# Performance work log

Hardware: AMD Instinct MI355X
Metric: run time of the kernel (lower is better)

## Reference

```python
import jax, jax.numpy as jnp
import numpy as np

NB, NC, NT = 64, 128, 6
NEURON = (25, 50, 100)
AXIS = 4
EPS = 1e-12


def _offdiag_idx(nc):
    # static [nc, nc-1] column indices of the off-diagonal entries per row
    idx = np.tile(np.arange(nc)[None, :], (nc, 1))
    mask = ~np.eye(nc, dtype=bool)
    return idx[mask].reshape(nc, nc - 1)


def setup_inputs() -> dict:
    key = jax.random.key(0)
    ks = jax.random.split(key, 8)
    P = NT * NT
    coords = jax.random.normal(ks[0], (NB, NC, 3), dtype=jnp.float32)
    atom_types = jax.random.randint(ks[1], (NC,), 0, NT)
    dims = [1] + list(NEURON)
    inp = {"coords": coords, "atom_types": atom_types}
    for i in range(3):
        bound = 1.0 / float(np.sqrt(dims[i]))
        inp[f"W{i+1}"] = jax.random.uniform(ks[2 + 2 * i], (P, dims[i + 1], dims[i]), jnp.float32, -bound, bound)
        inp[f"b{i+1}"] = jax.random.uniform(ks[3 + 2 * i], (P, dims[i + 1]), jnp.float32, -bound, bound)
    return inp


def _channel_dense(x, W, b, channels, res_mode):
    # x: [nb, Ppairs, in]; W[channels]: [Ppairs, out, in] (redundant per-pair gather, as in torch)
    y = jnp.einsum('bpi,poi->bpo', x, W[channels]) + b[channels]
    y = jnp.tanh(y)
    if res_mode == 1:
        y = y + x
    elif res_mode == 2:
        y = y + jnp.concatenate([x, x], axis=-1)
    return y


def _forward(coords, atom_types, W1, b1, W2, b2, W3, b3):
    nb, nc, _ = coords.shape
    idx = jnp.asarray(_offdiag_idx(nc))  # [nc, nc-1], static
    row = jnp.arange(nc)[:, None]

    rij = coords[:, :, None, :] - coords[:, None, :, :]          # [nb,nc,nc,3]
    rij = rij[:, row, idx]                                       # [nb,nc,nc-1,3] off-diagonal
    dij = jnp.linalg.norm(rij, axis=-1)                          # [nb,nc,nc-1]
    dinv = 1.0 / jnp.maximum(dij, EPS)
    loc_env_r = dinv
    loc_env_a = rij * (dinv * dinv)[..., None]                   # [nb,nc,nc-1,3]

    neighbor_types = atom_types[idx]                             # [nc,nc-1]
    channels = (atom_types[:, None] * NT + neighbor_types).reshape(-1)  # [nc*(nc-1)]

    x = loc_env_r.reshape(nb, -1, 1)                             # [nb,P,1]
    y = _channel_dense(x, W1, b1, channels, res_mode=0)          # 1 -> 25
    y = _channel_dense(y, W2, b2, channels, res_mode=2)          # 25 -> 50 (+concat res)
    y = _channel_dense(y, W3, b3, channels, res_mode=2)          # 50 -> 100 (+concat res)

    out = y.reshape(nb, nc, nc - 1, NEURON[-1])                  # [nb,nc,k,100]
    t1 = jnp.einsum('bnka,bnkf->bnaf', loc_env_a, out[..., :AXIS])   # [nb,nc,3,4]
    t2 = jnp.einsum('bnka,bnaf->bnkf', loc_env_a, t1)                # [nb,nc,k,4]
    res = jnp.einsum('bnkg,bnkf->bngf', out, t2)                     # [nb,nc,100,4]
    return res.reshape(nb, nc, -1)


def reference(coords, atom_types, W1, b1, W2, b2, W3, b3):
    return _forward(coords, atom_types, W1, b1, W2, b2, W3, b3)
```

## Files before the change

kernel.cpp:

```cpp
#include <hip/hip_runtime.h>

#define NBATCH 64
#define NCH    128
#define NTYPE  6
#define NK     127
#define N1     25
#define N2     50
#define N3     100
#define NAXIS  4
#define OUTPER 400
#define W2P    28
#define MAXKP  152
#define MAXC4  38

#define R5(M)  M(0) M(1) M(2) M(3) M(4)
#define R7(M)  M(0) M(1) M(2) M(3) M(4) M(5) M(6)
#define R12(M) M(0) M(1) M(2) M(3) M(4) M(5) M(6) M(7) M(8) M(9) M(10) M(11)
#define R25(M) M(0) M(1) M(2) M(3) M(4) M(5) M(6) M(7) M(8) M(9) M(10) M(11) M(12) \
               M(13) M(14) M(15) M(16) M(17) M(18) M(19) M(20) M(21) M(22) M(23) M(24)
#define R25A(M,a) M(a,0) M(a,1) M(a,2) M(a,3) M(a,4) M(a,5) M(a,6) M(a,7) M(a,8) M(a,9) \
               M(a,10) M(a,11) M(a,12) M(a,13) M(a,14) M(a,15) M(a,16) M(a,17) M(a,18) \
               M(a,19) M(a,20) M(a,21) M(a,22) M(a,23) M(a,24)
#define R50(M) R25(M) M(25) M(26) M(27) M(28) M(29) M(30) M(31) M(32) M(33) M(34) \
               M(35) M(36) M(37) M(38) M(39) M(40) M(41) M(42) M(43) M(44) M(45) \
               M(46) M(47) M(48) M(49)

__device__ __forceinline__ float tanh_fast(float x) {
    float e = __expf(2.0f * x);
    return 1.0f - 2.0f * __builtin_amdgcn_rcpf(e + 1.0f);
}

__global__ void k_transpose(const float* __restrict__ coords, float* __restrict__ ct) {
    int t = blockIdx.x * blockDim.x + threadIdx.x;
    if (t >= NBATCH * NCH * 3) return;
    int b  = t & (NBATCH - 1);
    int jd = t >> 6;
    int d  = jd % 3;
    int j  = jd / 3;
    ct[t] = coords[(b * NCH + j) * 3 + d];
}

__device__ __forceinline__ void sort_k_by_type(
    const int* __restrict__ types, int n, int* tysh, int* ks, int* bins, int tid, int nthr)
{
    for (int t = tid; t < NCH; t += nthr) tysh[t] = types[t];
    __syncthreads();
    if (tid == 0) {
        for (int t = 0; t < NTYPE; ++t) bins[t] = 0;
        for (int k = 0; k < NK; ++k) { int j = (k < n) ? k : k + 1; bins[tysh[j]]++; }
        int off = 0;
        for (int t = 0; t < NTYPE; ++t) { int c = bins[t]; bins[t] = off; off += c; }
        for (int k = 0; k < NK; ++k) { int j = (k < n) ? k : k + 1; ks[bins[tysh[j]]++] = k; }
    }
    __syncthreads();
}

__device__ __forceinline__ void sort_pad(
    const int* __restrict__ types, int n, int* tysh, int* ksp, int* chs, int* aux,
    int tid, int nthr)
{
    for (int t = tid; t < NCH; t += nthr) tysh[t] = types[t];
    __syncthreads();
    if (tid == 0) {
        int cnt[NTYPE], pos[NTYPE];
        for (int t = 0; t < NTYPE; ++t) cnt[t] = 0;
        for (int k = 0; k < NK; ++k) { int j = (k < n) ? k : k + 1; cnt[tysh[j]]++; }
        int c = 0;
        for (int t = 0; t < NTYPE; ++t) {
            pos[t] = c;
            int pc = (cnt[t] + 3) & ~3;
            for (int q = c >> 2; q < (c + pc) >> 2; ++q) chs[q] = t;
            for (int p = c + cnt[t]; p < c + pc; ++p) ksp[p] = -1;
            c += pc;
        }
        aux[0] = c >> 2;
        for (int k = 0; k < NK; ++k) { int j = (k < n) ? k : k + 1; ksp[pos[tysh[j]]++] = k; }
    }
    __syncthreads();
}

__global__ __launch_bounds__(256, 4) void k_mlp(
    const float* __restrict__ ct, const int* __restrict__ types,
    const float* __restrict__ W1, const float* __restrict__ B1,
    const float* __restrict__ W2, const float* __restrict__ B2,
    const float* __restrict__ W3, const float* __restrict__ B3,
    float* __restrict__ t1buf)
{
    __shared__ int ks[NK];
    __shared__ int tysh[NCH];
    __shared__ int bins[NTYPE];

    const int n  = blockIdx.x >> 2;
    const int qc = blockIdx.x & 3;
    const int w  = threadIdx.x >> 6;
    const int b  = threadIdx.x & 63;
    const int k0 = qc * 32 + w * 8;

    sort_k_by_type(types, n, tysh, ks, bins, threadIdx.x, 256);

    const float cx = ct[(n*3+0)*NBATCH + b];
    const float cy = ct[(n*3+1)*NBATCH + b];
    const float cz = ct[(n*3+2)*NBATCH + b];
    const int tn = __builtin_amdgcn_readfirstlane(tysh[n]);

    float t1a[12];
#define TIN(i) t1a[i] = 0.0f;
    R12(TIN)
#undef TIN

    for (int kk = 0; kk < 8; ++kk) {
        const int kidx = k0 + kk;
        if (kidx >= NK) break;
        const int sk = __builtin_amdgcn_readfirstlane(ks[kidx]);
        const int j  = (sk < n) ? sk : sk + 1;
        const int ch = __builtin_amdgcn_readfirstlane(tn * NTYPE + tysh[j]);

        const float dx = cx - ct[(j*3+0)*NBATCH + b];
        const float dy = cy - ct[(j*3+1)*NBATCH + b];
        const float dz = cz - ct[(j*3+2)*NBATCH + b];
        const float d2 = dx*dx + dy*dy + dz*dz;
        const float dd = sqrtf(d2);
        const float dinv = __builtin_amdgcn_rcpf(fmaxf(dd, 1e-12f));
        const float di2 = dinv * dinv;
        const float ax = dx * di2, ay = dy * di2, az = dz * di2;

        const float* w1r = W1 + ch * N1;
        const float* b1r = B1 + ch * N1;
        float y1[N1];
#define L1S(o) y1[o] = tanh_fast(fmaf(dinv, w1r[o], b1r[o]));
        R25(L1S)
#undef L1S

        const float* w2r = W2 + ch * (N2 * N1);
        const float* b2r = B2 + ch * N2;
        const float* w3r = W3 + ch * (N3 * N2);
        float zf[4];
        zf[0] = B3[ch*N3+0]; zf[1] = B3[ch*N3+1];
        zf[2] = B3[ch*N3+2]; zf[3] = B3[ch*N3+3];
        float r[4];
#define MLP2I(o,i) z = fmaf(w2r[(o)*N1+(i)], y1[i], z);
#define MLP2(o) { float z = b2r[o]; R25A(MLP2I,o) \
        float y2o = tanh_fast(z) + y1[(o)%N1]; \
        if ((o) < 4) r[(o)&3] = y2o; \
        zf[0] = fmaf(w3r[0*N2+(o)], y2o, zf[0]); \
        zf[1] = fmaf(w3r[1*N2+(o)], y2o, zf[1]); \
        zf[2] = fmaf(w3r[2*N2+(o)], y2o, zf[2]); \
        zf[3] = fmaf(w3r[3*N2+(o)], y2o, zf[3]); }
        R50(MLP2)
#undef MLP2
#undef MLP2I

#define O4F(f) { float o4 = tanh_fast(zf[f]) + r[f]; \
        t1a[0+(f)] = fmaf(ax, o4, t1a[0+(f)]); \
        t1a[4+(f)] = fmaf(ay, o4, t1a[4+(f)]); \
        t1a[8+(f)] = fmaf(az, o4, t1a[8+(f)]); }
        O4F(0) O4F(1) O4F(2) O4F(3)
#undef O4F
    }

    float* dst = t1buf + (n * 12) * NBATCH + b;
#define TAT(i) atomicAdd(dst + (i) * NBATCH, t1a[i]);
    R12(TAT)
#undef TAT
}

__global__ __launch_bounds__(512, 3) void k_res2(
    const float* __restrict__ ct, const int* __restrict__ types,
    const float* __restrict__ W1, const float* __restrict__ B1,
    const float* __restrict__ W2, const float* __restrict__ B2,
    const float* __restrict__ W3, const float* __restrict__ B3,
    const float* __restrict__ t1buf, float* __restrict__ out)
{
    __shared__ float y2t[4 * N2 * NBATCH];
    __shared__ float t2s[4 * NBATCH * NAXIS];
    __shared__ float w2s[N2 * W2P];
    __shared__ float w1s[N1], b1s[N1], b2s[N2];
    __shared__ int   ksp[MAXKP];
    __shared__ int   chs[MAXC4];
    __shared__ int   tysh[NCH];
    __shared__ int   aux[1];

    const int n    = blockIdx.x >> 2;
    const int gh   = (blockIdx.x >> 1) & 1;
    const int kh   = blockIdx.x & 1;
    const int w    = threadIdx.x >> 6;
    const int lane = threadIdx.x & 63;
    const int kk2  = w >> 1;
    const int h    = w & 1;
    const int tid  = threadIdx.x;

    sort_pad(types, n, tysh, ksp, chs, aux, tid, 512);
    const int nch4 = __builtin_amdgcn_readfirstlane(aux[0]);
    const int c_lo = kh ? (nch4 >> 1) : 0;
    const int c_hi = kh ? nch4 : (nch4 >> 1);

    const int tn = __builtin_amdgcn_readfirstlane(tysh[n]);

    float t1r[12];
#define T1L(i) t1r[i] = t1buf[(n*12 + (i))*NBATCH + lane];
    R12(T1L)
#undef T1L

    const int g0 = __builtin_amdgcn_readfirstlane(w * 7);
    int gg[7];
#define GGI(gi) gg[gi] = ((g0 + (gi)) < N2) ? (g0 + (gi)) : (N2 - 1);
    R7(GGI)
#undef GGI

    float racc[7][4];
#define RIN(gi) racc[gi][0]=0.f; racc[gi][1]=0.f; racc[gi][2]=0.f; racc[gi][3]=0.f;
    R7(RIN)
#undef RIN

    float b3v[7];
    int prevty = -1;

    for (int kc = c_lo; kc < c_hi; ++kc) {
        const int tj = __builtin_amdgcn_readfirstlane(chs[kc]);
        const int ch = tn * NTYPE + tj;
        if (tj != prevty) {
            for (int idx = tid; idx < N2*N1; idx += 512)
                w2s[(idx / N1) * W2P + (idx % N1)] = W2[ch*(N2*N1) + idx];
            if (tid < N1) { w1s[tid] = W1[ch*N1+tid]; b1s[tid] = B1[ch*N1+tid]; }
            if (tid < N2) b2s[tid] = B2[ch*N2+tid];
#define B3L(gi) b3v[gi] = B3[ch*N3 + gh*N2 + gg[gi]];
            R7(B3L)
#undef B3L
            prevty = tj;
            __syncthreads();
        }
        const int kb = kc * 4;
        {
            const int sk = __builtin_amdgcn_readfirstlane(ksp[kb + kk2]);
            if (sk >= 0) {
                const int j = (sk < n) ? sk : sk + 1;
                const float dx = ct[(n*3+0)*NBATCH + lane] - ct[(j*3+0)*NBATCH + lane];
                const float dy = ct[(n*3+1)*NBATCH + lane] - ct[(j*3+1)*NBATCH + lane];
                const float dz = ct[(n*3+2)*NBATCH + lane] - ct[(j*3+2)*NBATCH + lane];
                const float d2 = dx*dx + dy*dy + dz*dz;
                const float dd = sqrtf(d2);
                const float dinv = __builtin_amdgcn_rcpf(fmaxf(dd, 1e-12f));

                if (h == 0) {
                    const float di2 = dinv * dinv;
                    const float ax = dx * di2, ay = dy * di2, az = dz * di2;
#define T2W(f) t2s[(kk2*NBATCH + lane)*NAXIS + (f)] = \
                    ax*t1r[f] + ay*t1r[4+(f)] + az*t1r[8+(f)];
                    T2W(0) T2W(1) T2W(2) T2W(3)
#undef T2W
                }

                float y1[N1];
#define L1S(o) y1[o] = tanh_fast(fmaf(dinv, w1s[o], b1s[o]));
                R25(L1S)
#undef L1S
                const int ob = h * N1;
                float* y2w = &y2t[(kk2*N2 + ob)*NBATCH + lane];
#define P1Q(oi,q) { float4 wq = *(const float4*)&w2s[(ob+(oi))*W2P + (q)*4]; \
                    z = fmaf(wq.x, y1[(q)*4+0], z); z = fmaf(wq.y, y1[(q)*4+1], z); \
                    z = fmaf(wq.z, y1[(q)*4+2], z); z = fmaf(wq.w, y1[(q)*4+3], z); }
#define P1S(oi) { float z = b2s[ob+(oi)]; \
                  P1Q(oi,0) P1Q(oi,1) P1Q(oi,2) P1Q(oi,3) P1Q(oi,4) P1Q(oi,5) \
                  z = fmaf(w2s[(ob+(oi))*W2P + 24], y1[24], z); \
                  y2w[(oi)*NBATCH] = tanh_fast(z) + y1[oi]; }
                R25(P1S)
#undef P1S
#undef P1Q
            }
        }
        __syncthreads();
        const float* w3b = W3 + ch * (N3*N2) + (gh*N2) * N2;
        for (int kp = 0; kp < 2; ++kp) {
            const int skA = __builtin_amdgcn_readfirstlane(ksp[kb + kp*2 + 0]);
            const int skB = __builtin_amdgcn_readfirstlane(ksp[kb + kp*2 + 1]);
            if (skA < 0 && skB < 0) continue;
            const float* y2A = &y2t[((kp*2+0)*N2)*NBATCH + lane];
            const float* y2B = &y2t[((kp*2+1)*N2)*NBATCH + lane];
            float zA[7], zB[7];
#define ZIN(gi) zA[gi] = b3v[gi]; zB[gi] = b3v[gi];
            R7(ZIN)
#undef ZIN
            for (int ic = 0; ic < 10; ++ic) {
                const int io = ic * 5;
                float w35[7][5];
#define W35L(gi) w35[gi][0]=w3b[gg[gi]*N2+io+0]; w35[gi][1]=w3b[gg[gi]*N2+io+1]; \
                 w35[gi][2]=w3b[gg[gi]*N2+io+2]; w35[gi][3]=w3b[gg[gi]*N2+io+3]; \
                 w35[gi][4]=w3b[gg[gi]*N2+io+4];
                R7(W35L)
#undef W35L
                if (skA >= 0) {
                    float yv[5];
#define LDA(i) yv[i] = y2A[(io + (i))*NBATCH];
                    R5(LDA)
#undef LDA
#define FA(gi) zA[gi]=fmaf(w35[gi][0],yv[0],zA[gi]); zA[gi]=fmaf(w35[gi][1],yv[1],zA[gi]); \
               zA[gi]=fmaf(w35[gi][2],yv[2],zA[gi]); zA[gi]=fmaf(w35[gi][3],yv[3],zA[gi]); \
               zA[gi]=fmaf(w35[gi][4],yv[4],zA[gi]);
                    R7(FA)
#undef FA
                }
                if (skB >= 0) {
                    float yv[5];
#define LDB(i) yv[i] = y2B[(io + (i))*NBATCH];
                    R5(LDB)
#undef LDB
#define FB(gi) zB[gi]=fmaf(w35[gi][0],yv[0],zB[gi]); zB[gi]=fmaf(w35[gi][1],yv[1],zB[gi]); \
               zB[gi]=fmaf(w35[gi][2],yv[2],zB[gi]); zB[gi]=fmaf(w35[gi][3],yv[3],zB[gi]); \
               zB[gi]=fmaf(w35[gi][4],yv[4],zB[gi]);
                    R7(FB)
#undef FB
                }
            }
            if (skA >= 0) {
                const float4 t2v = *(const float4*)&t2s[((kp*2+0)*NBATCH + lane)*NAXIS];
#define PFA(gi) { float o3 = tanh_fast(zA[gi]) + y2A[gg[gi]*NBATCH]; \
                  racc[gi][0] = fmaf(o3, t2v.x, racc[gi][0]); \
                  racc[gi][1] = fmaf(o3, t2v.y, racc[gi][1]); \
                  racc[gi][2] = fmaf(o3, t2v.z, racc[gi][2]); \
                  racc[gi][3] = fmaf(o3, t2v.w, racc[gi][3]); }
                R7(PFA)
#undef PFA
            }
            if (skB >= 0) {
                const float4 t2v = *(const float4*)&t2s[((kp*2+1)*NBATCH + lane)*NAXIS];
#define PFB(gi) { float o3 = tanh_fast(zB[gi]) + y2B[gg[gi]*NBATCH]; \
                  racc[gi][0] = fmaf(o3, t2v.x, racc[gi][0]); \
                  racc[gi][1] = fmaf(o3, t2v.y, racc[gi][1]); \
                  racc[gi][2] = fmaf(o3, t2v.z, racc[gi][2]); \
                  racc[gi][3] = fmaf(o3, t2v.w, racc[gi][3]); }
                R7(PFB)
#undef PFB
            }
        }
        __syncthreads();
    }

#define PST(gi) if (g0 + (gi) < N2) { \
        float* dp = &out[(lane*NCH + n)*OUTPER + (gh*N2 + g0 + (gi))*NAXIS]; \
        atomicAdd(dp + 0, racc[gi][0]); \
        atomicAdd(dp + 1, racc[gi][1]); \
        atomicAdd(dp + 2, racc[gi][2]); \
        atomicAdd(dp + 3, racc[gi][3]); }
    R7(PST)
#undef PST
}

extern "C" void kernel_launch(void* const* d_in, const int* in_sizes, int n_in,
                              void* d_out, int out_size, void* d_ws, size_t ws_size,
                              hipStream_t stream) {
    const float* coords = (const float*)d_in[0];
    const int*   types  = (const int*)d_in[1];
    const float* W1 = (const float*)d_in[2];
    const float* B1 = (const float*)d_in[3];
    const float* W2 = (const float*)d_in[4];
    const float* B2 = (const float*)d_in[5];
    const float* W3 = (const float*)d_in[6];
    const float* B3 = (const float*)d_in[7];
    float* out = (float*)d_out;

    float* t1buf = (float*)d_ws;
    float* ct    = t1buf + NCH * 12 * NBATCH;

    hipMemsetAsync(t1buf, 0, (size_t)NCH * 12 * NBATCH * sizeof(float), stream);
    hipMemsetAsync(out, 0, (size_t)out_size * sizeof(float), stream);

    k_transpose<<<(NBATCH*NCH*3 + 255)/256, 256, 0, stream>>>(coords, ct);
    k_mlp <<<NCH*4, 256, 0, stream>>>(ct, types, W1,B1,W2,B2,W3,B3, t1buf);
    k_res2<<<NCH*4, 512, 0, stream>>>(ct, types, W1,B1,W2,B2,W3,B3, t1buf, out);
}
```

Measured before the change: 829.2 us.

## Compute both output halves per block and split neighbor chunks four ways

Each k_res2 block now computes both halves of the 100-wide layer-3 output instead of one, and the grid index selects one of four neighbor-chunk quarters instead of a half/half split. This removes the duplicated layer-1/layer-2 evaluation and W2 staging that the two output-half blocks previously repeated for the same neighbors. In exchange it doubles accumulator and bias registers, so launch bounds drop to 2 blocks per CU, lowering occupancy. Atomic output stores per block also double.

New measurement: 1.186 ms. 43.0% more time.

```diff
diff --git a/kernel.cpp b/kernel.cpp
--- a/kernel.cpp
+++ b/kernel.cpp
@@ -15,6 +15,7 @@
 
 #define R5(M)  M(0) M(1) M(2) M(3) M(4)
 #define R7(M)  M(0) M(1) M(2) M(3) M(4) M(5) M(6)
+#define R7A(M,a) M(a,0) M(a,1) M(a,2) M(a,3) M(a,4) M(a,5) M(a,6)
 #define R12(M) M(0) M(1) M(2) M(3) M(4) M(5) M(6) M(7) M(8) M(9) M(10) M(11)
 #define R25(M) M(0) M(1) M(2) M(3) M(4) M(5) M(6) M(7) M(8) M(9) M(10) M(11) M(12) \
                M(13) M(14) M(15) M(16) M(17) M(18) M(19) M(20) M(21) M(22) M(23) M(24)
@@ -164,7 +165,7 @@
 #undef TAT
 }
 
-__global__ __launch_bounds__(512, 3) void k_res2(
+__global__ __launch_bounds__(512, 2) void k_res2(
     const float* __restrict__ ct, const int* __restrict__ types,
     const float* __restrict__ W1, const float* __restrict__ B1,
     const float* __restrict__ W2, const float* __restrict__ B2,
@@ -181,8 +182,7 @@
     __shared__ int   aux[1];
 
     const int n    = blockIdx.x >> 2;
-    const int gh   = (blockIdx.x >> 1) & 1;
-    const int kh   = blockIdx.x & 1;
+    const int kh   = blockIdx.x & 3;
     const int w    = threadIdx.x >> 6;
     const int lane = threadIdx.x & 63;
     const int kk2  = w >> 1;
@@ -191,8 +191,8 @@
 
     sort_pad(types, n, tysh, ksp, chs, aux, tid, 512);
     const int nch4 = __builtin_amdgcn_readfirstlane(aux[0]);
-    const int c_lo = kh ? (nch4 >> 1) : 0;
-    const int c_hi = kh ? nch4 : (nch4 >> 1);
+    const int c_lo = (nch4 * kh) >> 2;
+    const int c_hi = (nch4 * (kh + 1)) >> 2;
 
     const int tn = __builtin_amdgcn_readfirstlane(tysh[n]);
 
@@ -207,12 +207,13 @@
     R7(GGI)
 #undef GGI
 
-    float racc[7][4];
-#define RIN(gi) racc[gi][0]=0.f; racc[gi][1]=0.f; racc[gi][2]=0.f; racc[gi][3]=0.f;
+    float racc0[7][4], racc1[7][4];
+#define RIN(gi) racc0[gi][0]=0.f; racc0[gi][1]=0.f; racc0[gi][2]=0.f; racc0[gi][3]=0.f; \
+                racc1[gi][0]=0.f; racc1[gi][1]=0.f; racc1[gi][2]=0.f; racc1[gi][3]=0.f;
     R7(RIN)
 #undef RIN
 
-    float b3v[7];
+    float b3v0[7], b3v1[7];
     int prevty = -1;
 
     for (int kc = c_lo; kc < c_hi; ++kc) {
@@ -223,7 +224,7 @@
                 w2s[(idx / N1) * W2P + (idx % N1)] = W2[ch*(N2*N1) + idx];
             if (tid < N1) { w1s[tid] = W1[ch*N1+tid]; b1s[tid] = B1[ch*N1+tid]; }
             if (tid < N2) b2s[tid] = B2[ch*N2+tid];
-#define B3L(gi) b3v[gi] = B3[ch*N3 + gh*N2 + gg[gi]];
+#define B3L(gi) b3v0[gi] = B3[ch*N3 + gg[gi]]; b3v1[gi] = B3[ch*N3 + N2 + gg[gi]];
             R7(B3L)
 #undef B3L
             prevty = tj;
@@ -269,78 +270,88 @@
             }
         }
         __syncthreads();
-        const float* w3b = W3 + ch * (N3*N2) + (gh*N2) * N2;
-        for (int kp = 0; kp < 2; ++kp) {
-            const int skA = __builtin_amdgcn_readfirstlane(ksp[kb + kp*2 + 0]);
-            const int skB = __builtin_amdgcn_readfirstlane(ksp[kb + kp*2 + 1]);
-            if (skA < 0 && skB < 0) continue;
-            const float* y2A = &y2t[((kp*2+0)*N2)*NBATCH + lane];
-            const float* y2B = &y2t[((kp*2+1)*N2)*NBATCH + lane];
-            float zA[7], zB[7];
-#define ZIN(gi) zA[gi] = b3v[gi]; zB[gi] = b3v[gi];
-            R7(ZIN)
-#undef ZIN
-            for (int ic = 0; ic < 10; ++ic) {
-                const int io = ic * 5;
-                float w35[7][5];
-#define W35L(gi) w35[gi][0]=w3b[gg[gi]*N2+io+0]; w35[gi][1]=w3b[gg[gi]*N2+io+1]; \
-                 w35[gi][2]=w3b[gg[gi]*N2+io+2]; w35[gi][3]=w3b[gg[gi]*N2+io+3]; \
-                 w35[gi][4]=w3b[gg[gi]*N2+io+4];
-                R7(W35L)
-#undef W35L
-                if (skA >= 0) {
-                    float yv[5];
+        const float* w3b0 = W3 + ch * (N3*N2);
+        const float* w3b1 = W3 + ch * (N3*N2) + N2*N2;
+#define ZIN(s,gi) zA[gi] = b3v##s[gi]; zB[gi] = b3v##s[gi];
+#define W35L(s,gi) w35[gi][0]=w3b##s[gg[gi]*N2+io+0]; w35[gi][1]=w3b##s[gg[gi]*N2+io+1]; \
+                   w35[gi][2]=w3b##s[gg[gi]*N2+io+2]; w35[gi][3]=w3b##s[gg[gi]*N2+io+3]; \
+                   w35[gi][4]=w3b##s[gg[gi]*N2+io+4];
 #define LDA(i) yv[i] = y2A[(io + (i))*NBATCH];
-                    R5(LDA)
-#undef LDA
+#define LDB(i) yv[i] = y2B[(io + (i))*NBATCH];
 #define FA(gi) zA[gi]=fmaf(w35[gi][0],yv[0],zA[gi]); zA[gi]=fmaf(w35[gi][1],yv[1],zA[gi]); \
                zA[gi]=fmaf(w35[gi][2],yv[2],zA[gi]); zA[gi]=fmaf(w35[gi][3],yv[3],zA[gi]); \
                zA[gi]=fmaf(w35[gi][4],yv[4],zA[gi]);
-                    R7(FA)
-#undef FA
-                }
-                if (skB >= 0) {
-                    float yv[5];
-#define LDB(i) yv[i] = y2B[(io + (i))*NBATCH];
-                    R5(LDB)
-#undef LDB
 #define FB(gi) zB[gi]=fmaf(w35[gi][0],yv[0],zB[gi]); zB[gi]=fmaf(w35[gi][1],yv[1],zB[gi]); \
                zB[gi]=fmaf(w35[gi][2],yv[2],zB[gi]); zB[gi]=fmaf(w35[gi][3],yv[3],zB[gi]); \
                zB[gi]=fmaf(w35[gi][4],yv[4],zB[gi]);
-                    R7(FB)
+#define PFA(s,gi) { float o3 = tanh_fast(zA[gi]) + y2A[gg[gi]*NBATCH]; \
+                  racc##s[gi][0] = fmaf(o3, t2v.x, racc##s[gi][0]); \
+                  racc##s[gi][1] = fmaf(o3, t2v.y, racc##s[gi][1]); \
+                  racc##s[gi][2] = fmaf(o3, t2v.z, racc##s[gi][2]); \
+                  racc##s[gi][3] = fmaf(o3, t2v.w, racc##s[gi][3]); }
+#define PFB(s,gi) { float o3 = tanh_fast(zB[gi]) + y2B[gg[gi]*NBATCH]; \
+                  racc##s[gi][0] = fmaf(o3, t2v.x, racc##s[gi][0]); \
+                  racc##s[gi][1] = fmaf(o3, t2v.y, racc##s[gi][1]); \
+                  racc##s[gi][2] = fmaf(o3, t2v.z, racc##s[gi][2]); \
+                  racc##s[gi][3] = fmaf(o3, t2v.w, racc##s[gi][3]); }
+#define PH2(s) \
+        for (int kp = 0; kp < 2; ++kp) { \
+            const int skA = __builtin_amdgcn_readfirstlane(ksp[kb + kp*2 + 0]); \
+            const int skB = __builtin_amdgcn_readfirstlane(ksp[kb + kp*2 + 1]); \
+            if (skA < 0 && skB < 0) continue; \
+            const float* y2A = &y2t[((kp*2+0)*N2)*NBATCH + lane]; \
+            const float* y2B = &y2t[((kp*2+1)*N2)*NBATCH + lane]; \
+            float zA[7], zB[7]; \
+            R7A(ZIN,s) \
+            for (int ic = 0; ic < 10; ++ic) { \
+                const int io = ic * 5; \
+                float w35[7][5]; \
+                R7A(W35L,s) \
+                if (skA >= 0) { \
+                    float yv[5]; \
+                    R5(LDA) \
+                    R7(FA) \
+                } \
+                if (skB >= 0) { \
+                    float yv[5]; \
+                    R5(LDB) \
+                    R7(FB) \
+                } \
+            } \
+            if (skA >= 0) { \
+                const float4 t2v = *(const float4*)&t2s[((kp*2+0)*NBATCH + lane)*NAXIS]; \
+                R7A(PFA,s) \
+            } \
+            if (skB >= 0) { \
+                const float4 t2v = *(const float4*)&t2s[((kp*2+1)*NBATCH + lane)*NAXIS]; \
+                R7A(PFB,s) \
+            } \
+        }
+        PH2(0)
+        PH2(1)
+#undef PH2
+#undef PFB
+#undef PFA
 #undef FB
-                }
-            }
-            if (skA >= 0) {
-                const float4 t2v = *(const float4*)&t2s[((kp*2+0)*NBATCH + lane)*NAXIS];
-#define PFA(gi) { float o3 = tanh_fast(zA[gi]) + y2A[gg[gi]*NBATCH]; \
-                  racc[gi][0] = fmaf(o3, t2v.x, racc[gi][0]); \
-                  racc[gi][1] = fmaf(o3, t2v.y, racc[gi][1]); \
-                  racc[gi][2] = fmaf(o3, t2v.z, racc[gi][2]); \
-                  racc[gi][3] = fmaf(o3, t2v.w, racc[gi][3]); }
-                R7(PFA)
-#undef PFA
-            }
-            if (skB >= 0) {
-                const float4 t2v = *(const float4*)&t2s[((kp*2+1)*NBATCH + lane)*NAXIS];
-#define PFB(gi) { float o3 = tanh_fast(zB[gi]) + y2B[gg[gi]*NBATCH]; \
-                  racc[gi][0] = fmaf(o3, t2v.x, racc[gi][0]); \
-                  racc[gi][1] = fmaf(o3, t2v.y, racc[gi][1]); \
-                  racc[gi][2] = fmaf(o3, t2v.z, racc[gi][2]); \
-                  racc[gi][3] = fmaf(o3, t2v.w, racc[gi][3]); }
-                R7(PFB)
-#undef PFB
-            }
-        }
+#undef FA
+#undef LDB
+#undef LDA
+#undef W35L
+#undef ZIN
         __syncthreads();
     }
 
 #define PST(gi) if (g0 + (gi) < N2) { \
-        float* dp = &out[(lane*NCH + n)*OUTPER + (gh*N2 + g0 + (gi))*NAXIS]; \
-        atomicAdd(dp + 0, racc[gi][0]); \
-        atomicAdd(dp + 1, racc[gi][1]); \
-        atomicAdd(dp + 2, racc[gi][2]); \
-        atomicAdd(dp + 3, racc[gi][3]); }
+        float* dp0 = &out[(lane*NCH + n)*OUTPER + (g0 + (gi))*NAXIS]; \
+        atomicAdd(dp0 + 0, racc0[gi][0]); \
+        atomicAdd(dp0 + 1, racc0[gi][1]); \
+        atomicAdd(dp0 + 2, racc0[gi][2]); \
+        atomicAdd(dp0 + 3, racc0[gi][3]); \
+        float* dp1 = &out[(lane*NCH + n)*OUTPER + (N2 + g0 + (gi))*NAXIS]; \
+        atomicAdd(dp1 + 0, racc1[gi][0]); \
+        atomicAdd(dp1 + 1, racc1[gi][1]); \
+        atomicAdd(dp1 + 2, racc1[gi][2]); \
+        atomicAdd(dp1 + 3, racc1[gi][3]); }
     R7(PST)
 #undef PST
 }
```
